# Kernel optimization log

Hardware: AMD Instinct MI355X
Metric: run time of the kernel (lower is better)

Reference implementation:

```python
import jax, jax.numpy as jnp
import numpy as np

N = 100000      # nodes
E = 3200000     # edges (avg degree 32)
DIN, DH, DOUT = 256, 256, 64
K = 10          # propagation hops


def _uniform(key, shape, fan_in):
    b = 1.0 / np.sqrt(fan_in)
    return jax.random.uniform(key, shape, jnp.float32, -b, b)


def setup_inputs() -> dict:
    key = jax.random.key(0)
    ks = jax.random.split(key, 8)
    x = jax.random.normal(ks[0], (N, DIN), jnp.float32)
    edge_index = jax.random.randint(ks[1], (2, E), 0, N, dtype=jnp.int64)
    W1 = _uniform(ks[2], (DIN, DH), DIN)
    b1 = _uniform(ks[3], (DH,), DIN)
    W2 = _uniform(ks[4], (DH, DOUT), DH)
    b2 = _uniform(ks[5], (DOUT,), DH)
    proj_w = _uniform(ks[6], (DOUT,), DOUT)
    proj_b = _uniform(ks[7], (), DOUT)
    return {"x": x, "edge_index": edge_index, "W1": W1, "b1": b1,
            "W2": W2, "b2": b2, "proj_w": proj_w, "proj_b": proj_b}


def _gcn_norm(edge_index, num_nodes):
    # add self-loops with weight 1, symmetric normalization deg^-1/2 A deg^-1/2
    loops = jnp.arange(num_nodes, dtype=edge_index.dtype)
    row = jnp.concatenate([edge_index[0], loops])
    col = jnp.concatenate([edge_index[1], loops])
    w = jnp.ones(row.shape[0], jnp.float32)
    deg = jax.ops.segment_sum(w, col, num_segments=num_nodes)
    dinv = jnp.where(deg > 0, jax.lax.rsqrt(deg), 0.0)
    norm = dinv[row] * dinv[col]  # edge weight is 1
    return row, col, norm


def reference(x, edge_index, W1, b1, W2, b2, proj_w, proj_b):
    h = jax.nn.relu(x @ W1 + b1)
    h = h @ W2 + b2                               # [N, DOUT]
    row, col, norm = _gcn_norm(edge_index, N)
    preds = [h]
    for _ in range(K):
        h = jax.ops.segment_sum(norm[:, None] * h[row], col, num_segments=N)
        preds.append(h)
    pps = jnp.stack(preds, axis=1)                # [N, K+1, DOUT]
    score = jax.nn.sigmoid(pps @ proj_w + proj_b) # [N, K+1]
    out = jnp.einsum('nk,nkc->nc', score, pps)    # adaptive hop pooling
    return out
```

## Files before the change

### kernel.cpp

```cpp
#include <hip/hip_runtime.h>
#include <hip/hip_bf16.h>
#include <math.h>


#define WAVE 64
#define NBLK 1024
#define RS 520

__device__ inline float bf2f(unsigned short u) {
    union { unsigned int i; float f; } v; v.i = ((unsigned int)u) << 16; return v.f;
}
__device__ inline unsigned short f2bf(float f) {
    __hip_bfloat16 b = __float2bfloat16(f);
    union { __hip_bfloat16 b; unsigned short u; } v; v.b = b; return v.u;
}

typedef __attribute__((ext_vector_type(8))) short bf16x8;
typedef __attribute__((ext_vector_type(16))) float f32x16;

__global__ void detect_kernel(const unsigned* __restrict__ e, int* __restrict__ sflag) {
    __shared__ int any;
    if (threadIdx.x == 0) any = 0;
    __syncthreads();
    unsigned nz = 0;
    int t = threadIdx.x;
    for (int i = 0; i < 8; ++i) nz |= e[(size_t)(t * 8 + i) * 2 + 1];
    if (nz) atomicOr(&any, 1);
    __syncthreads();
    if (t == 0) *sflag = any ? 1 : 2;
}

__global__ void passA_kernel(const int* __restrict__ eidx, const int* __restrict__ sflag,
                             int* __restrict__ blk_cnt, int E, int NB, int EPB) {
    __shared__ int lh[512];
    int t = threadIdx.x, blk = blockIdx.x;
    for (int i = t; i < NB; i += 256) lh[i] = 0;
    __syncthreads();
    int s = *sflag;
    int base = blk * EPB;
    int end = base + EPB; if (end > E) end = E;
    for (int e = base + t; e < end; e += 256) {
        int c = eidx[(size_t)s * (size_t)(E + e)];
        atomicAdd(&lh[c >> 8], 1);
    }
    __syncthreads();
    for (int i = t; i < NB; i += 256)
        blk_cnt[(size_t)i * NBLK + blk] = lh[i];
}

__global__ void scan1_kernel(const int* __restrict__ in, int* __restrict__ out,
                             int* __restrict__ bsums, int n) {
    __shared__ int s[256];
    int t = threadIdx.x;
    int idx = blockIdx.x * 1024 + t * 4;
    int x0 = (idx + 0 < n) ? in[idx + 0] : 0;
    int x1 = (idx + 1 < n) ? in[idx + 1] : 0;
    int x2 = (idx + 2 < n) ? in[idx + 2] : 0;
    int x3 = (idx + 3 < n) ? in[idx + 3] : 0;
    int lsum = x0 + x1 + x2 + x3;
    s[t] = lsum;
    __syncthreads();
    for (int o = 1; o < 256; o <<= 1) {
        int v = (t >= o) ? s[t - o] : 0;
        __syncthreads();
        if (t >= o) s[t] += v;
        __syncthreads();
    }
    int excl = s[t] - lsum;
    if (idx + 0 < n) out[idx + 0] = excl;
    if (idx + 1 < n) out[idx + 1] = excl + x0;
    if (idx + 2 < n) out[idx + 2] = excl + x0 + x1;
    if (idx + 3 < n) out[idx + 3] = excl + x0 + x1 + x2;
    if (t == 255) bsums[blockIdx.x] = s[255];
}

__global__ void scan2g_kernel(int* __restrict__ bsums, int nb) {
    __shared__ int part[256];
    int t = threadIdx.x;
    int v[4]; int run = 0;
    #pragma unroll
    for (int j = 0; j < 4; ++j) {
        int i = t * 4 + j;
        int x = (i < nb) ? bsums[i] : 0;
        v[j] = run; run += x;
    }
    part[t] = run;
    __syncthreads();
    for (int o = 1; o < 256; o <<= 1) {
        int x = (t >= o) ? part[t - o] : 0;
        __syncthreads();
        if (t >= o) part[t] += x;
        __syncthreads();
    }
    int excl = part[t] - run;
    #pragma unroll
    for (int j = 0; j < 4; ++j) {
        int i = t * 4 + j;
        if (i < nb) bsums[i] = excl + v[j];
    }
}

__global__ void scan3_kernel(int* __restrict__ arr, const int* __restrict__ bsums,
                             int n, int total) {
    int t = threadIdx.x;
    int idx = blockIdx.x * 1024 + t * 4;
    int add = bsums[blockIdx.x];
    #pragma unroll
    for (int i = 0; i < 4; ++i)
        if (idx + i < n) arr[idx + i] += add;
    if (blockIdx.x == 0 && t == 0) arr[n] = total;
}

__global__ void passB_kernel(const int* __restrict__ eidx, const int* __restrict__ sflag,
                             const int* __restrict__ pbase, int2* __restrict__ pairs,
                             int E, int NB, int EPB) {
    __shared__ int lcur[512];
    int t = threadIdx.x, blk = blockIdx.x;
    for (int i = t; i < NB; i += 256) lcur[i] = pbase[(size_t)i * NBLK + blk];
    __syncthreads();
    int s = *sflag;
    int base = blk * EPB;
    int end = base + EPB; if (end > E) end = E;
    for (int e = base + t; e < end; e += 256) {
        int r = eidx[(size_t)s * (size_t)e];
        int c = eidx[(size_t)s * (size_t)(E + e)];
        int pos = atomicAdd(&lcur[c >> 8], 1);
        pairs[pos] = make_int2(r, c);
    }
}

__global__ void passD_kernel(const int2* __restrict__ pairs, const int* __restrict__ pbase,
                             int* __restrict__ cnt, int N) {
    __shared__ int lcnt[256];
    int b = blockIdx.x, t = threadIdx.x;
    lcnt[t] = 0;
    __syncthreads();
    int w0 = pbase[(size_t)b * NBLK], w1 = pbase[(size_t)(b + 1) * NBLK];
    for (int i = w0 + t; i < w1; i += 256)
        atomicAdd(&lcnt[pairs[i].y & 255], 1);
    __syncthreads();
    int node = b * 256 + t;
    if (node < N) cnt[node] = lcnt[t];
}

__global__ void dinv_kernel(const int* __restrict__ cnt, float* __restrict__ dinv, int n) {
    int i = blockIdx.x * blockDim.x + threadIdx.x;
    if (i < n) dinv[i] = rsqrtf((float)(cnt[i] + 1));
}

__global__ void passC_kernel(const int2* __restrict__ pairs, const int* __restrict__ pbase,
                             const int* __restrict__ offs, int* __restrict__ csr_src,
                             int N) {
    __shared__ int lcur[256];
    int b = blockIdx.x, t = threadIdx.x;
    int node = b * 256 + t;
    lcur[t] = (node < N) ? offs[node] : 0;
    __syncthreads();
    int w0 = pbase[(size_t)b * NBLK], w1 = pbase[(size_t)(b + 1) * NBLK];
    for (int i = w0 + t; i < w1; i += 256) {
        int2 p = pairs[i];
        int pos = atomicAdd(&lcur[p.y & 255], 1);
        csr_src[pos] = p.x;
    }
}

__global__ void wconv_kernel(const float* __restrict__ W, unsigned short* __restrict__ Wt,
                             int K, int Nn) {
    int i = blockIdx.x * blockDim.x + threadIdx.x;
    if (i >= K * Nn) return;
    int n = i / K, k = i - n * K;
    Wt[(size_t)n * K + k] = f2bf(W[(size_t)k * Nn + n]);
}

__global__ __launch_bounds__(256, 4) void mlp_fused(
        const float* __restrict__ x,
        const unsigned short* __restrict__ W1t,
        const float* __restrict__ b1,
        const unsigned short* __restrict__ W2t,
        const float* __restrict__ b2,
        const float* __restrict__ dinv,
        const float* __restrict__ pw, const float* __restrict__ pb,
        float* __restrict__ out, unsigned short* __restrict__ g,
        int M) {
    __shared__ unsigned short xfrag[4 * RS];
    __shared__ unsigned short h1frag[32 * RS];

    int tid = threadIdx.x;
    int wave = tid >> 6, lane = tid & 63;
    int half = lane >> 5, l31 = lane & 31;
    int rt = wave & 1;
    int cw = wave >> 1;
    int bm = blockIdx.x * 64;

    f32x16 acc1[4] = {};

    float4 xv[2];
    #pragma unroll
    for (int i = 0; i < 2; ++i) {
        int f = i * 256 + tid;
        int row = f >> 3, c4 = (f & 7) * 4;
        int grow = bm + row;
        xv[i] = (grow < M) ? *(const float4*)(x + (size_t)grow * 256 + c4)
                           : make_float4(0.f, 0.f, 0.f, 0.f);
    }

    for (int it = 0; it < 8; ++it) {
        #pragma unroll
        for (int i = 0; i < 2; ++i) {
            int f = i * 256 + tid;
            int row = f >> 3, c4 = (f & 7) * 4;
            int region = c4 >> 3, off = c4 & 7;
            ushort4 u;
            u.x = f2bf(xv[i].x); u.y = f2bf(xv[i].y);
            u.z = f2bf(xv[i].z); u.w = f2bf(xv[i].w);
            *(ushort4*)&xfrag[region * RS + row * 8 + off] = u;
        }
        __syncthreads();
        if (it < 7) {
            int k0 = (it + 1) * 32;
            #pragma unroll
            for (int i = 0; i < 2; ++i) {
                int f = i * 256 + tid;
                int row = f >> 3, c4 = (f & 7) * 4;
                int grow = bm + row;
                xv[i] = (grow < M) ? *(const float4*)(x + (size_t)grow * 256 + k0 + c4)
                                   : make_float4(0.f, 0.f, 0.f, 0.f);
            }
        }
        int kg = it * 32 + half * 8;
        #pragma unroll
        for (int s = 0; s < 2; ++s) {
            bf16x8 a = *(bf16x8*)&xfrag[(s * 2 + half) * RS + (rt * 32 + l31) * 8];
            #pragma unroll
            for (int j = 0; j < 4; ++j) {
                int ch = cw * 128 + j * 32 + l31;
                bf16x8 b = *(const bf16x8*)(W1t + (size_t)ch * 256 + kg + s * 16);
                acc1[j] = __builtin_amdgcn_mfma_f32_32x32x16_bf16(a, b, acc1[j], 0, 0, 0);
            }
        }
        __syncthreads();
    }

    #pragma unroll
    for (int j = 0; j < 4; ++j) {
        int ch = cw * 128 + j * 32 + l31;
        float bb = b1[ch];
        int region = ch >> 3, off = ch & 7;
        #pragma unroll
        for (int reg = 0; reg < 16; ++reg) {
            int rowin = (reg & 3) + 8 * (reg >> 2) + 4 * half;
            int row = rt * 32 + rowin;
            float v = fmaxf(acc1[j][reg] + bb, 0.f);
            h1frag[region * RS + row * 8 + off] = f2bf(v);
        }
    }
    __syncthreads();

    if (wave < 2) {
        f32x16 acc2[2] = {};
        #pragma unroll
        for (int s = 0; s < 16; ++s) {
            bf16x8 a = *(bf16x8*)&h1frag[(s * 2 + half) * RS + (wave * 32 + l31) * 8];
            #pragma unroll
            for (int j = 0; j < 2; ++j) {
                bf16x8 b = *(const bf16x8*)(W2t + (size_t)(j * 32 + l31) * 256 + s * 16 + half * 8);
                acc2[j] = __builtin_amdgcn_mfma_f32_32x32x16_bf16(a, b, acc2[j], 0, 0, 0);
            }
        }
        float bb0 = b2[l31], bb1 = b2[32 + l31];
        float pw0 = pw[l31], pw1 = pw[32 + l31];
        float pbv = pb[0];
        #pragma unroll
        for (int reg = 0; reg < 16; ++reg) {
            int rowin = (reg & 3) + 8 * (reg >> 2) + 4 * half;
            int row = bm + wave * 32 + rowin;
            float h0 = acc2[0][reg] + bb0;
            float h1v = acc2[1][reg] + bb1;
            float d = h0 * pw0 + h1v * pw1;
            d += __shfl_xor(d, 1, 64);
            d += __shfl_xor(d, 2, 64);
            d += __shfl_xor(d, 4, 64);
            d += __shfl_xor(d, 8, 64);
            d += __shfl_xor(d, 16, 64);
            float sg = 1.f / (1.f + __expf(-(d + pbv)));
            if (row < M) {
                float dv = dinv[row];
                out[(size_t)row * 64 + l31]      = sg * h0;
                out[(size_t)row * 64 + 32 + l31] = sg * h1v;
                g[(size_t)row * 64 + l31]        = f2bf(dv * h0);
                g[(size_t)row * 64 + 32 + l31]   = f2bf(dv * h1v);
            }
        }
    }
}

__global__ void spmm_kernel(const int* __restrict__ offs, const int* __restrict__ src,
                            const float* __restrict__ dinv,
                            const __hip_bfloat16* __restrict__ gin,
                            __hip_bfloat16* __restrict__ gout,
                            float* __restrict__ out,
                            const float* __restrict__ pw, const float* __restrict__ pb,
                            int n) {
    int wid = (blockIdx.x * blockDim.x + threadIdx.x) >> 6;
    int lane = threadIdx.x & 63;
    if (wid >= n) return;
    int c = __builtin_amdgcn_readfirstlane(wid);
    int e = __builtin_amdgcn_readfirstlane(offs[c]);
    int eend = __builtin_amdgcn_readfirstlane(offs[c + 1]);
    float acc = 0.f;
    while (e < eend && (e & 3)) {
        acc += __bfloat162float(gin[(size_t)src[e] * 64 + lane]);
        ++e;
    }
    for (; e + 7 < eend; e += 8) {
        int4 sa = *(const int4*)(src + e);
        int4 sb = *(const int4*)(src + e + 4);
        float v0 = __bfloat162float(gin[(size_t)sa.x * 64 + lane]);
        float v1 = __bfloat162float(gin[(size_t)sa.y * 64 + lane]);
        float v2 = __bfloat162float(gin[(size_t)sa.z * 64 + lane]);
        float v3 = __bfloat162float(gin[(size_t)sa.w * 64 + lane]);
        float v4 = __bfloat162float(gin[(size_t)sb.x * 64 + lane]);
        float v5 = __bfloat162float(gin[(size_t)sb.y * 64 + lane]);
        float v6 = __bfloat162float(gin[(size_t)sb.z * 64 + lane]);
        float v7 = __bfloat162float(gin[(size_t)sb.w * 64 + lane]);
        acc += ((v0 + v1) + (v2 + v3)) + ((v4 + v5) + (v6 + v7));
    }
    for (; e + 3 < eend; e += 4) {
        int4 sa = *(const int4*)(src + e);
        float v0 = __bfloat162float(gin[(size_t)sa.x * 64 + lane]);
        float v1 = __bfloat162float(gin[(size_t)sa.y * 64 + lane]);
        float v2 = __bfloat162float(gin[(size_t)sa.z * 64 + lane]);
        float v3 = __bfloat162float(gin[(size_t)sa.w * 64 + lane]);
        acc += (v0 + v1) + (v2 + v3);
    }
    for (; e < eend; ++e) acc += __bfloat162float(gin[(size_t)src[e] * 64 + lane]);

    float dc = dinv[c];
    float h = dc * (acc + __bfloat162float(gin[(size_t)c * 64 + lane]));
    gout[(size_t)c * 64 + lane] = __float2bfloat16(dc * h);
    float d = h * pw[lane];
    #pragma unroll
    for (int o = 32; o > 0; o >>= 1) d += __shfl_xor(d, o, 64);
    float sg = 1.f / (1.f + __expf(-(d + pb[0])));
    out[(size_t)c * 64 + lane] += sg * h;
}

extern "C" void kernel_launch(void* const* d_in, const int* in_sizes, int n_in,
                              void* d_out, int out_size, void* d_ws, size_t ws_size,
                              hipStream_t stream) {
    const float* x  = (const float*)d_in[0];
    const int* eidx = (const int*)d_in[1];
    const float* W1 = (const float*)d_in[2];
    const float* b1 = (const float*)d_in[3];
    const float* W2 = (const float*)d_in[4];
    const float* b2 = (const float*)d_in[5];
    const float* pw = (const float*)d_in[6];
    const float* pb = (const float*)d_in[7];
    float* out = (float*)d_out;

    const int N = in_sizes[0] / 256;
    const int E = in_sizes[1] / 2;
    const int NB = (N + 255) >> 8;
    const int EPB = (E + NBLK - 1) / NBLK;
    const int M = NB * NBLK;

    size_t woff = 0;
    auto alloc = [&](size_t bytes) -> void* {
        void* p = (char*)d_ws + woff;
        woff += (bytes + 255) & ~(size_t)255;
        return p;
    };
    int*   sflag   = (int*)alloc(4);
    int*   cnt     = (int*)alloc((size_t)N * 4);
    float* dinv    = (float*)alloc((size_t)N * 4);
    int*   offs    = (int*)alloc(((size_t)N + 1) * 4);
    int*   bsums   = (int*)alloc(1024 * 4);
    int*   bsums2  = (int*)alloc(1024 * 4);
    int*   pbase   = (int*)alloc(((size_t)M + 1) * 4);
    int*   csr_src = (int*)alloc((size_t)E * 4);
    int2*  pairs   = (int2*)alloc((size_t)E * 8);
    unsigned short* W1t = (unsigned short*)alloc((size_t)256 * 256 * 2);
    unsigned short* W2t = (unsigned short*)alloc((size_t)64 * 256 * 2);
    __hip_bfloat16* gA = (__hip_bfloat16*)alloc((size_t)N * 64 * 2);
    __hip_bfloat16* gB = (__hip_bfloat16*)alloc((size_t)N * 64 * 2);

    detect_kernel<<<1, 256, 0, stream>>>((const unsigned*)eidx, sflag);

    passA_kernel<<<NBLK, 256, 0, stream>>>(eidx, sflag, pbase, E, NB, EPB);
    int nb2 = (M + 1023) / 1024;
    scan1_kernel<<<nb2, 256, 0, stream>>>(pbase, pbase, bsums2, M);
    scan2g_kernel<<<1, 256, 0, stream>>>(bsums2, nb2);
    scan3_kernel<<<nb2, 256, 0, stream>>>(pbase, bsums2, M, E);
    passB_kernel<<<NBLK, 256, 0, stream>>>(eidx, sflag, pbase, pairs, E, NB, EPB);
    passD_kernel<<<NB, 256, 0, stream>>>(pairs, pbase, cnt, N);
    dinv_kernel<<<(N + 255) / 256, 256, 0, stream>>>(cnt, dinv, N);
    int nb1 = (N + 1023) / 1024;
    scan1_kernel<<<nb1, 256, 0, stream>>>(cnt, offs, bsums, N);
    scan2g_kernel<<<1, 256, 0, stream>>>(bsums, nb1);
    scan3_kernel<<<nb1, 256, 0, stream>>>(offs, bsums, N, E);
    passC_kernel<<<NB, 256, 0, stream>>>(pairs, pbase, offs, csr_src, N);

    wconv_kernel<<<(256 * 256 + 255) / 256, 256, 0, stream>>>(W1, W1t, 256, 256);
    wconv_kernel<<<(64 * 256 + 255) / 256, 256, 0, stream>>>(W2, W2t, 256, 64);
    int gb = (N + 63) / 64;
    mlp_fused<<<gb, 256, 0, stream>>>(x, W1t, b1, W2t, b2, dinv, pw, pb,
                                      out, (unsigned short*)gA, N);

    int nwb = (N + 3) / 4;
    __hip_bfloat16* gin = gA;
    __hip_bfloat16* gout = gB;
    for (int k = 0; k < 10; ++k) {
        spmm_kernel<<<nwb, 256, 0, stream>>>(offs, csr_src, dinv, gin, gout, out, pw, pb, N);
        __hip_bfloat16* t = gin; gin = gout; gout = t;
    }
}
```

Baseline: 1.112 ms.

## Transpose bucket-count layout, pre-fragment MLP weights, split second GEMM across waves

The per-block bucket counts are now stored block-major, so the consumer passes walk contiguous per-block segments, with one thread running serially through each segment. Both weight matrices are converted into an 8-wide k-fragment layout so the MFMA operand loads read contiguous memory. The second GEMM now runs on all four waves instead of two, each computing one 32x32 tile, and the projection dot-product is reduced across waves through shared memory. The trade-off is that the serial per-thread segment loops in the CSR build may read memory less coalesced and balance load worse, and the MLP epilogue gains an extra barrier.

```diff
diff --git a/kernel.cpp b/kernel.cpp
--- a/kernel.cpp
+++ b/kernel.cpp
@@ -45,7 +45,7 @@
     }
     __syncthreads();
     for (int i = t; i < NB; i += 256)
-        blk_cnt[(size_t)i * NBLK + blk] = lh[i];
+        blk_cnt[(size_t)blk * NB + i] = lh[i];
 }
 
 __global__ void scan1_kernel(const int* __restrict__ in, int* __restrict__ out,
@@ -116,7 +116,7 @@
                              int E, int NB, int EPB) {
     __shared__ int lcur[512];
     int t = threadIdx.x, blk = blockIdx.x;
-    for (int i = t; i < NB; i += 256) lcur[i] = pbase[(size_t)i * NBLK + blk];
+    for (int i = t; i < NB; i += 256) lcur[i] = pbase[(size_t)blk * NB + i];
     __syncthreads();
     int s = *sflag;
     int base = blk * EPB;
@@ -130,14 +130,17 @@
 }
 
 __global__ void passD_kernel(const int2* __restrict__ pairs, const int* __restrict__ pbase,
-                             int* __restrict__ cnt, int N) {
+                             int* __restrict__ cnt, int N, int NB) {
     __shared__ int lcnt[256];
     int b = blockIdx.x, t = threadIdx.x;
     lcnt[t] = 0;
     __syncthreads();
-    int w0 = pbase[(size_t)b * NBLK], w1 = pbase[(size_t)(b + 1) * NBLK];
-    for (int i = w0 + t; i < w1; i += 256)
-        atomicAdd(&lcnt[pairs[i].y & 255], 1);
+    for (int blk = t; blk < NBLK; blk += 256) {
+        int w0 = pbase[(size_t)blk * NB + b];
+        int w1 = pbase[(size_t)blk * NB + b + 1];
+        for (int i = w0; i < w1; ++i)
+            atomicAdd(&lcnt[pairs[i].y & 255], 1);
+    }
     __syncthreads();
     int node = b * 256 + t;
     if (node < N) cnt[node] = lcnt[t];
@@ -150,33 +153,36 @@
 
 __global__ void passC_kernel(const int2* __restrict__ pairs, const int* __restrict__ pbase,
                              const int* __restrict__ offs, int* __restrict__ csr_src,
-                             int N) {
+                             int N, int NB) {
     __shared__ int lcur[256];
     int b = blockIdx.x, t = threadIdx.x;
     int node = b * 256 + t;
     lcur[t] = (node < N) ? offs[node] : 0;
     __syncthreads();
-    int w0 = pbase[(size_t)b * NBLK], w1 = pbase[(size_t)(b + 1) * NBLK];
-    for (int i = w0 + t; i < w1; i += 256) {
-        int2 p = pairs[i];
-        int pos = atomicAdd(&lcur[p.y & 255], 1);
-        csr_src[pos] = p.x;
-    }
-}
-
-__global__ void wconv_kernel(const float* __restrict__ W, unsigned short* __restrict__ Wt,
+    for (int blk = t; blk < NBLK; blk += 256) {
+        int w0 = pbase[(size_t)blk * NB + b];
+        int w1 = pbase[(size_t)blk * NB + b + 1];
+        for (int i = w0; i < w1; ++i) {
+            int2 p = pairs[i];
+            int pos = atomicAdd(&lcur[p.y & 255], 1);
+            csr_src[pos] = p.x;
+        }
+    }
+}
+
+__global__ void wconv_kernel(const float* __restrict__ W, unsigned short* __restrict__ Wf,
                              int K, int Nn) {
     int i = blockIdx.x * blockDim.x + threadIdx.x;
     if (i >= K * Nn) return;
-    int n = i / K, k = i - n * K;
-    Wt[(size_t)n * K + k] = f2bf(W[(size_t)k * Nn + n]);
+    int k = i / Nn, n = i - k * Nn;
+    Wf[(size_t)(k >> 3) * Nn * 8 + n * 8 + (k & 7)] = f2bf(W[i]);
 }
 
 __global__ __launch_bounds__(256, 4) void mlp_fused(
         const float* __restrict__ x,
-        const unsigned short* __restrict__ W1t,
+        const unsigned short* __restrict__ W1f,
         const float* __restrict__ b1,
-        const unsigned short* __restrict__ W2t,
+        const unsigned short* __restrict__ W2f,
         const float* __restrict__ b2,
         const float* __restrict__ dinv,
         const float* __restrict__ pw, const float* __restrict__ pb,
@@ -184,6 +190,7 @@
         int M) {
     __shared__ unsigned short xfrag[4 * RS];
     __shared__ unsigned short h1frag[32 * RS];
+    __shared__ float pools[2][2][2][16];
 
     int tid = threadIdx.x;
     int wave = tid >> 6, lane = tid & 63;
@@ -227,14 +234,14 @@
                                    : make_float4(0.f, 0.f, 0.f, 0.f);
             }
         }
-        int kg = it * 32 + half * 8;
         #pragma unroll
         for (int s = 0; s < 2; ++s) {
+            int region = it * 4 + s * 2 + half;
             bf16x8 a = *(bf16x8*)&xfrag[(s * 2 + half) * RS + (rt * 32 + l31) * 8];
             #pragma unroll
             for (int j = 0; j < 4; ++j) {
                 int ch = cw * 128 + j * 32 + l31;
-                bf16x8 b = *(const bf16x8*)(W1t + (size_t)ch * 256 + kg + s * 16);
+                bf16x8 b = *(const bf16x8*)(W1f + (size_t)region * 2048 + ch * 8);
                 acc1[j] = __builtin_amdgcn_mfma_f32_32x32x16_bf16(a, b, acc1[j], 0, 0, 0);
             }
         }
@@ -256,40 +263,43 @@
     }
     __syncthreads();
 
-    if (wave < 2) {
-        f32x16 acc2[2] = {};
-        #pragma unroll
-        for (int s = 0; s < 16; ++s) {
-            bf16x8 a = *(bf16x8*)&h1frag[(s * 2 + half) * RS + (wave * 32 + l31) * 8];
-            #pragma unroll
-            for (int j = 0; j < 2; ++j) {
-                bf16x8 b = *(const bf16x8*)(W2t + (size_t)(j * 32 + l31) * 256 + s * 16 + half * 8);
-                acc2[j] = __builtin_amdgcn_mfma_f32_32x32x16_bf16(a, b, acc2[j], 0, 0, 0);
-            }
-        }
-        float bb0 = b2[l31], bb1 = b2[32 + l31];
-        float pw0 = pw[l31], pw1 = pw[32 + l31];
-        float pbv = pb[0];
-        #pragma unroll
-        for (int reg = 0; reg < 16; ++reg) {
-            int rowin = (reg & 3) + 8 * (reg >> 2) + 4 * half;
-            int row = bm + wave * 32 + rowin;
-            float h0 = acc2[0][reg] + bb0;
-            float h1v = acc2[1][reg] + bb1;
-            float d = h0 * pw0 + h1v * pw1;
-            d += __shfl_xor(d, 1, 64);
-            d += __shfl_xor(d, 2, 64);
-            d += __shfl_xor(d, 4, 64);
-            d += __shfl_xor(d, 8, 64);
-            d += __shfl_xor(d, 16, 64);
-            float sg = 1.f / (1.f + __expf(-(d + pbv)));
-            if (row < M) {
-                float dv = dinv[row];
-                out[(size_t)row * 64 + l31]      = sg * h0;
-                out[(size_t)row * 64 + 32 + l31] = sg * h1v;
-                g[(size_t)row * 64 + l31]        = f2bf(dv * h0);
-                g[(size_t)row * 64 + 32 + l31]   = f2bf(dv * h1v);
-            }
+    int rt2 = wave >> 1, ct2 = wave & 1;
+    f32x16 acc2 = {};
+    #pragma unroll
+    for (int s = 0; s < 16; ++s) {
+        bf16x8 a = *(bf16x8*)&h1frag[(s * 2 + half) * RS + (rt2 * 32 + l31) * 8];
+        bf16x8 b = *(const bf16x8*)(W2f + (size_t)(s * 2 + half) * 512 + (ct2 * 32 + l31) * 8);
+        acc2 = __builtin_amdgcn_mfma_f32_32x32x16_bf16(a, b, acc2, 0, 0, 0);
+    }
+
+    float bb = b2[ct2 * 32 + l31];
+    float pwv = pw[ct2 * 32 + l31];
+    float pbv = pb[0];
+    float hreg[16];
+    #pragma unroll
+    for (int reg = 0; reg < 16; ++reg) {
+        float h = acc2[reg] + bb;
+        hreg[reg] = h;
+        float d = h * pwv;
+        d += __shfl_xor(d, 1, 64);
+        d += __shfl_xor(d, 2, 64);
+        d += __shfl_xor(d, 4, 64);
+        d += __shfl_xor(d, 8, 64);
+        d += __shfl_xor(d, 16, 64);
+        if (l31 == 0) pools[rt2][ct2][half][reg] = d;
+    }
+    __syncthreads();
+    #pragma unroll
+    for (int reg = 0; reg < 16; ++reg) {
+        int rowin = (reg & 3) + 8 * (reg >> 2) + 4 * half;
+        int row = bm + rt2 * 32 + rowin;
+        float d = pools[rt2][0][half][reg] + pools[rt2][1][half][reg];
+        float sg = 1.f / (1.f + __expf(-(d + pbv)));
+        float h = hreg[reg];
+        if (row < M) {
+            float dv = dinv[row];
+            out[(size_t)row * 64 + ct2 * 32 + l31] = sg * h;
+            g[(size_t)row * 64 + ct2 * 32 + l31]   = f2bf(dv * h);
         }
     }
 }
@@ -379,8 +389,8 @@
     int*   pbase   = (int*)alloc(((size_t)M + 1) * 4);
     int*   csr_src = (int*)alloc((size_t)E * 4);
     int2*  pairs   = (int2*)alloc((size_t)E * 8);
-    unsigned short* W1t = (unsigned short*)alloc((size_t)256 * 256 * 2);
-    unsigned short* W2t = (unsigned short*)alloc((size_t)64 * 256 * 2);
+    unsigned short* W1f = (unsigned short*)alloc((size_t)256 * 256 * 2);
+    unsigned short* W2f = (unsigned short*)alloc((size_t)64 * 256 * 2);
     __hip_bfloat16* gA = (__hip_bfloat16*)alloc((size_t)N * 64 * 2);
     __hip_bfloat16* gB = (__hip_bfloat16*)alloc((size_t)N * 64 * 2);
 
@@ -392,18 +402,18 @@
     scan2g_kernel<<<1, 256, 0, stream>>>(bsums2, nb2);
     scan3_kernel<<<nb2, 256, 0, stream>>>(pbase, bsums2, M, E);
     passB_kernel<<<NBLK, 256, 0, stream>>>(eidx, sflag, pbase, pairs, E, NB, EPB);
-    passD_kernel<<<NB, 256, 0, stream>>>(pairs, pbase, cnt, N);
+    passD_kernel<<<NB, 256, 0, stream>>>(pairs, pbase, cnt, N, NB);
     dinv_kernel<<<(N + 255) / 256, 256, 0, stream>>>(cnt, dinv, N);
     int nb1 = (N + 1023) / 1024;
     scan1_kernel<<<nb1, 256, 0, stream>>>(cnt, offs, bsums, N);
     scan2g_kernel<<<1, 256, 0, stream>>>(bsums, nb1);
     scan3_kernel<<<nb1, 256, 0, stream>>>(offs, bsums, N, E);
-    passC_kernel<<<NB, 256, 0, stream>>>(pairs, pbase, offs, csr_src, N);
-
-    wconv_kernel<<<(256 * 256 + 255) / 256, 256, 0, stream>>>(W1, W1t, 256, 256);
-    wconv_kernel<<<(64 * 256 + 255) / 256, 256, 0, stream>>>(W2, W2t, 256, 64);
+    passC_kernel<<<NB, 256, 0, stream>>>(pairs, pbase, offs, csr_src, N, NB);
+
+    wconv_kernel<<<(256 * 256 + 255) / 256, 256, 0, stream>>>(W1, W1f, 256, 256);
+    wconv_kernel<<<(64 * 256 + 255) / 256, 256, 0, stream>>>(W2, W2f, 256, 64);
     int gb = (N + 63) / 64;
-    mlp_fused<<<gb, 256, 0, stream>>>(x, W1t, b1, W2t, b2, dinv, pw, pb,
+    mlp_fused<<<gb, 256, 0, stream>>>(x, W1f, b1, W2f, b2, dinv, pw, pb,
                                       out, (unsigned short*)gA, N);
 
     int nwb = (N + 3) / 4;
```

Measured after the change: 1.100 ms. About the same (-1.1%).
